# Optimization experiments

Hardware: AMD Instinct MI355X
Metric: run time of the kernel (lower is better)

## Reference

```python
import jax, jax.numpy as jnp
import numpy as np

NUM_HEADS = 12
HEAD_DIM = 64
DIM = 768
ATTN_DIM = 768
SEQ = 4096


def _rotate_half(t):
    # split last dim in halves: (x1, x2) -> (-x2, x1)
    x1, x2 = jnp.split(t, 2, axis=-1)
    return jnp.concatenate([-x2, x1], axis=-1)


def _apply_rope(t, freqs):
    # t: [B,H,L,d], freqs: [1,1,L,d]
    return t * jnp.cos(freqs) + _rotate_half(t) * jnp.sin(freqs)


def setup_inputs() -> dict:
    key = jax.random.key(0)
    ks = jax.random.split(key, 8)
    x = jax.random.normal(ks[0], (1, SEQ, DIM), dtype=jnp.float32)
    # standard rotary frequencies: theta = pos * inv_freq, concatenated twice to head_dim
    inv_freq = 1.0 / (10000.0 ** (jnp.arange(0, HEAD_DIM, 2, dtype=jnp.float32) / HEAD_DIM))
    pos = jnp.arange(SEQ, dtype=jnp.float32)
    ang = pos[:, None] * inv_freq[None, :]                      # [L, d/2]
    rope = jnp.concatenate([ang, ang], axis=-1)[None, None]     # [1,1,L,d]
    s = 0.02
    Wq = jax.random.normal(ks[1], (ATTN_DIM, DIM), dtype=jnp.float32) * s
    Wk = jax.random.normal(ks[2], (ATTN_DIM, DIM), dtype=jnp.float32) * s
    Wv = jax.random.normal(ks[3], (ATTN_DIM, DIM), dtype=jnp.float32) * s
    Wo = jax.random.normal(ks[4], (DIM, ATTN_DIM), dtype=jnp.float32) * s
    bo = jnp.zeros((DIM,), dtype=jnp.float32)
    gamma = jnp.ones((DIM,), dtype=jnp.float32)
    beta = jnp.zeros((DIM,), dtype=jnp.float32)
    return {"x": x, "Wq": Wq, "Wk": Wk, "Wv": Wv, "Wo": Wo, "bo": bo,
            "gamma": gamma, "beta": beta, "rope": rope}


def reference(x, Wq, Wk, Wv, Wo, bo, gamma, beta, rope):
    B, L, D = x.shape
    residual = x
    # pre-LayerNorm
    mu = jnp.mean(x, axis=-1, keepdims=True)
    var = jnp.mean((x - mu) ** 2, axis=-1, keepdims=True)
    xn = (x - mu) * jax.lax.rsqrt(var + 1e-5) * gamma + beta

    def heads(t):  # [B,L,attn_dim] -> [B,H,L,d]
        return t.reshape(B, L, NUM_HEADS, HEAD_DIM).transpose(0, 2, 1, 3)

    q = heads(xn @ Wq.T)
    k = heads(xn @ Wk.T)
    v = heads(xn @ Wv.T)
    q = _apply_rope(q, rope)
    k = _apply_rope(k, rope)
    v = _apply_rope(v, rope)

    scale = HEAD_DIM ** -0.5
    dots = jnp.einsum('bhid,bhjd->bhij', q, k) * scale
    # causal mask: positions j > i masked
    i = jnp.arange(L)
    mask = i[:, None] < i[None, :]  # True where future
    neg = -jnp.finfo(dots.dtype).max
    dots = jnp.where(mask[None, None], neg, dots)
    attn_map = jax.nn.softmax(dots, axis=-1)

    o = jnp.einsum('bhij,bhjd->bhid', attn_map, v)
    o = o.transpose(0, 2, 1, 3).reshape(B, L, ATTN_DIM)
    out = o @ Wo.T + bo + residual
    return out, attn_map, dots
```

## Files before the change

kernel.cpp:

```cpp
#include <hip/hip_runtime.h>
#include <hip/hip_bf16.h>
#include <cfloat>
#include <cmath>

#define SEQ 4096
#define DIM 768
#define NH 12
#define HD 64
#define NEG_MASK (-0x1.FEp+127f)

typedef __attribute__((ext_vector_type(8))) short short8_t;
typedef __attribute__((ext_vector_type(4))) float f32x4;

static __device__ __forceinline__ unsigned short f2bf(float f) {
  __hip_bfloat16 h = __float2bfloat16(f);
  unsigned short u;
  __builtin_memcpy(&u, &h, 2);
  return u;
}

static __device__ __forceinline__ void st_nt(float* p, f32x4 v) {
  __builtin_nontemporal_store(v, (f32x4*)p);
}
static __device__ __forceinline__ void st_nt1(float* p, float v) {
  __builtin_nontemporal_store(v, p);
}
static __device__ __forceinline__ f32x4 ld_lds4(const float* p) {
  return *(const f32x4*)p;
}

__global__ __launch_bounds__(256) void ln_kernel(const float* __restrict__ x,
    const float* __restrict__ gamma, const float* __restrict__ beta,
    unsigned short* __restrict__ xnb) {
  int row = blockIdx.x;
  const float* xr = x + (size_t)row * DIM;
  int t = threadIdx.x;
  float v0 = xr[t], v1 = xr[t + 256], v2 = xr[t + 512];
  float s = v0 + v1 + v2;
  float s2 = v0 * v0 + v1 * v1 + v2 * v2;
  for (int off = 32; off > 0; off >>= 1) {
    s += __shfl_down(s, off, 64);
    s2 += __shfl_down(s2, off, 64);
  }
  __shared__ float red[2][4];
  int wid = t >> 6;
  if ((t & 63) == 0) { red[0][wid] = s; red[1][wid] = s2; }
  __syncthreads();
  s = red[0][0] + red[0][1] + red[0][2] + red[0][3];
  s2 = red[1][0] + red[1][1] + red[1][2] + red[1][3];
  float mu = s * (1.0f / DIM);
  float var = s2 * (1.0f / DIM) - mu * mu;
  float rstd = rsqrtf(var + 1e-5f);
  unsigned short* xo = xnb + (size_t)row * DIM;
  xo[t]       = f2bf((v0 - mu) * rstd * gamma[t]       + beta[t]);
  xo[t + 256] = f2bf((v1 - mu) * rstd * gamma[t + 256] + beta[t + 256]);
  xo[t + 512] = f2bf((v2 - mu) * rstd * gamma[t + 512] + beta[t + 512]);
}

__global__ __launch_bounds__(256) void wcvt_kernel(const float* __restrict__ w0,
    const float* __restrict__ w1, const float* __restrict__ w2, const float* __restrict__ w3,
    unsigned short* __restrict__ o0, unsigned short* __restrict__ o1,
    unsigned short* __restrict__ o2, unsigned short* __restrict__ o3) {
  const float* src; unsigned short* dst;
  switch (blockIdx.y) {
    case 0: src = w0; dst = o0; break;
    case 1: src = w1; dst = o1; break;
    case 2: src = w2; dst = o2; break;
    default: src = w3; dst = o3; break;
  }
  size_t base = ((size_t)blockIdx.x * 256 + threadIdx.x) * 8;
  float4 a = *(const float4*)(src + base);
  float4 b = *(const float4*)(src + base + 4);
  ushort4 ua, ub;
  ua.x = f2bf(a.x); ua.y = f2bf(a.y); ua.z = f2bf(a.z); ua.w = f2bf(a.w);
  ub.x = f2bf(b.x); ub.y = f2bf(b.y); ub.z = f2bf(b.z); ub.w = f2bf(b.w);
  *(ushort4*)(dst + base) = ua;
  *(ushort4*)(dst + base + 4) = ub;
}

__global__ __launch_bounds__(256) void qkv_kernel(const unsigned short* __restrict__ xnb,
    const unsigned short* __restrict__ wqb, const unsigned short* __restrict__ wkb,
    const unsigned short* __restrict__ wvb, const float* __restrict__ ropes,
    unsigned short* __restrict__ qb, unsigned short* __restrict__ kb,
    unsigned short* __restrict__ vbT) {
  int z = blockIdx.z;
  const unsigned short* W = (z == 0) ? wqb : (z == 1) ? wkb : wvb;
  int h = blockIdx.y;
  int n0 = h * 64;
  int tid = threadIdx.x;
  int w = tid >> 6, l = tid & 63;
  int col_l = l & 15, rowg = l >> 4, kgrp = rowg * 8;
  int mbase = blockIdx.x * 64 + w * 16;

  f32x4 acc[4];
  #pragma unroll
  for (int g = 0; g < 4; g++) acc[g] = (f32x4){0.f, 0.f, 0.f, 0.f};

  for (int k0 = 0; k0 < DIM; k0 += 32) {
    short8_t a = *(const short8_t*)(xnb + (size_t)(mbase + col_l) * DIM + k0 + kgrp);
    #pragma unroll
    for (int g = 0; g < 4; g++) {
      short8_t bw = *(const short8_t*)(W + (size_t)(n0 + g * 16 + col_l) * DIM + k0 + kgrp);
      acc[g] = __builtin_amdgcn_mfma_f32_16x16x32_bf16(a, bw, acc[g], 0, 0, 0);
    }
  }

  float res[4][4];
  #pragma unroll
  for (int g = 0; g < 4; g++) {
    int d = g * 16 + col_l;
    #pragma unroll
    for (int r = 0; r < 4; r++) {
      int m = mbase + rowg * 4 + r;
      float f = ropes[(size_t)m * HD + d];
      float val = acc[g][r];
      float oth = acc[g ^ 2][r];
      float rot = (g < 2) ? -oth : oth;
      res[g][r] = val * cosf(f) + rot * sinf(f);
    }
  }

  if (z < 2) {
    unsigned short* dst = (z == 0) ? qb : kb;
    #pragma unroll
    for (int g = 0; g < 4; g++) {
      int d = g * 16 + col_l;
      #pragma unroll
      for (int r = 0; r < 4; r++)
        dst[((size_t)h * SEQ + mbase + rowg * 4 + r) * HD + d] = f2bf(res[g][r]);
    }
  } else {
    #pragma unroll
    for (int g = 0; g < 4; g++) {
      int d = g * 16 + col_l;
      ushort4 u;
      u.x = f2bf(res[g][0]); u.y = f2bf(res[g][1]);
      u.z = f2bf(res[g][2]); u.w = f2bf(res[g][3]);
      *(ushort4*)(vbT + ((size_t)h * HD + d) * SEQ + mbase + rowg * 4) = u;
    }
  }
}

__global__ __launch_bounds__(256, 4) void attn_fused(
    const unsigned short* __restrict__ qb, const unsigned short* __restrict__ kb,
    const unsigned short* __restrict__ vbT,
    float* __restrict__ dots, float* __restrict__ attnp, unsigned short* __restrict__ ob) {
  int bid = blockIdx.x;
  int g_ = (bid & 7) * 384 + (bid >> 3);
  int h = g_ >> 8;
  int band = 255 - (g_ & 255);
  int i0 = band * 16;
  int jd = i0 >> 6;
  int tid = threadIdx.x;
  int w = tid >> 6, l = tid & 63;
  int col_l = l & 15, rg = l >> 4, kgrp = rg * 8;

  const unsigned short* qh = qb + (size_t)h * SEQ * HD;
  const unsigned short* kh = kb + (size_t)h * SEQ * HD;
  const unsigned short* vh = vbT + (size_t)h * HD * SEQ;
  size_t obase = (size_t)h * SEQ * SEQ;

  __shared__ float pt[4][16][68];
  __shared__ float stats[4][16];

  const unsigned short* qrow = qh + (size_t)(i0 + col_l) * HD + kgrp;
  short8_t aq0 = *(const short8_t*)(qrow);
  short8_t aq1 = *(const short8_t*)(qrow + 32);

  float lsum[4];
  #pragma unroll
  for (int r = 0; r < 4; r++) lsum[r] = 0.f;

  for (int jt = w; jt <= jd; jt += 4) {
    int j0 = jt * 64;
    f32x4 acc[4];
    #pragma unroll
    for (int b = 0; b < 4; b++) {
      const unsigned short* kr = kh + (size_t)(j0 + b * 16 + col_l) * HD + kgrp;
      short8_t bk0 = *(const short8_t*)(kr);
      short8_t bk1 = *(const short8_t*)(kr + 32);
      f32x4 z = {0.f, 0.f, 0.f, 0.f};
      acc[b] = __builtin_amdgcn_mfma_f32_16x16x32_bf16(aq0, bk0, z, 0, 0, 0);
      acc[b] = __builtin_amdgcn_mfma_f32_16x16x32_bf16(aq1, bk1, acc[b], 0, 0, 0);
    }
    bool diag = (jt == jd);
    #pragma unroll
    for (int b = 0; b < 4; b++) {
      int j = j0 + b * 16 + col_l;
      #pragma unroll
      for (int r = 0; r < 4; r++) {
        float s = acc[b][r] * 0.125f;
        acc[b][r] = (diag && j > i0 + rg * 4 + r) ? NEG_MASK : s;
      }
    }
    #pragma unroll
    for (int r = 0; r < 4; r++) {
      lsum[r] += __expf(acc[0][r]) + __expf(acc[1][r]) +
                 __expf(acc[2][r]) + __expf(acc[3][r]);
    }
    #pragma unroll
    for (int b = 0; b < 4; b++) {
      float* dp = dots + obase + (size_t)(i0 + rg * 4) * SEQ + j0 + b * 16 + col_l;
      #pragma unroll
      for (int r = 0; r < 4; r++)
        st_nt1(dp + (size_t)r * SEQ, acc[b][r]);
    }
  }

  #pragma unroll
  for (int r = 0; r < 4; r++) {
    #pragma unroll
    for (int off = 1; off < 16; off <<= 1)
      lsum[r] += __shfl_xor(lsum[r], off, 16);
  }
  if (col_l == 0) {
    #pragma unroll
    for (int r = 0; r < 4; r++)
      stats[w][rg * 4 + r] = lsum[r];
  }
  __syncthreads();
  float rl_[4];
  #pragma unroll
  for (int r = 0; r < 4; r++) {
    int row = rg * 4 + r;
    rl_[r] = 1.0f / (stats[0][row] + stats[1][row] + stats[2][row] + stats[3][row]);
  }

  f32x4 o[4];
  #pragma unroll
  for (int dg = 0; dg < 4; dg++) o[dg] = (f32x4){0.f, 0.f, 0.f, 0.f};

  for (int jt = w; jt <= jd; jt += 4) {
    int j0 = jt * 64;
    f32x4 acc[4];
    #pragma unroll
    for (int b = 0; b < 4; b++) {
      const unsigned short* kr = kh + (size_t)(j0 + b * 16 + col_l) * HD + kgrp;
      short8_t bk0 = *(const short8_t*)(kr);
      short8_t bk1 = *(const short8_t*)(kr + 32);
      f32x4 z = {0.f, 0.f, 0.f, 0.f};
      acc[b] = __builtin_amdgcn_mfma_f32_16x16x32_bf16(aq0, bk0, z, 0, 0, 0);
      acc[b] = __builtin_amdgcn_mfma_f32_16x16x32_bf16(aq1, bk1, acc[b], 0, 0, 0);
    }
    bool diag = (jt == jd);
    #pragma unroll
    for (int b = 0; b < 4; b++) {
      int j = j0 + b * 16 + col_l;
      #pragma unroll
      for (int r = 0; r < 4; r++) {
        float s = acc[b][r] * 0.125f;
        s = (diag && j > i0 + rg * 4 + r) ? NEG_MASK : s;
        float p = __expf(s) * rl_[r];
        acc[b][r] = p;
        pt[w][rg * 4 + r][b * 16 + col_l] = p;
      }
    }
    #pragma unroll
    for (int b = 0; b < 4; b++) {
      float* ap = attnp + obase + (size_t)(i0 + rg * 4) * SEQ + j0 + b * 16 + col_l;
      #pragma unroll
      for (int r = 0; r < 4; r++)
        st_nt1(ap + (size_t)r * SEQ, acc[b][r]);
    }
    short8_t pa[2];
    #pragma unroll
    for (int ks = 0; ks < 2; ks++) {
      const float* src = &pt[w][col_l][ks * 32 + kgrp];
      f32x4 x0 = ld_lds4(src);
      f32x4 x1 = ld_lds4(src + 4);
      short8_t t;
      t[0] = (short)f2bf(x0.x); t[1] = (short)f2bf(x0.y);
      t[2] = (short)f2bf(x0.z); t[3] = (short)f2bf(x0.w);
      t[4] = (short)f2bf(x1.x); t[5] = (short)f2bf(x1.y);
      t[6] = (short)f2bf(x1.z); t[7] = (short)f2bf(x1.w);
      pa[ks] = t;
    }
    #pragma unroll
    for (int dg = 0; dg < 4; dg++) {
      const unsigned short* vr = vh + (size_t)(dg * 16 + col_l) * SEQ + j0 + kgrp;
      short8_t bv0 = *(const short8_t*)(vr);
      short8_t bv1 = *(const short8_t*)(vr + 32);
      o[dg] = __builtin_amdgcn_mfma_f32_16x16x32_bf16(pa[0], bv0, o[dg], 0, 0, 0);
      o[dg] = __builtin_amdgcn_mfma_f32_16x16x32_bf16(pa[1], bv1, o[dg], 0, 0, 0);
    }
  }

  {
    int c0 = (jd + 1) * 64;
    int nf4 = (SEQ - c0) >> 2;
    if (nf4 > 0) {
      f32x4 dm = (f32x4){NEG_MASK, NEG_MASK, NEG_MASK, NEG_MASK};
      f32x4 zz = (f32x4){0.f, 0.f, 0.f, 0.f};
      for (int r16 = 0; r16 < 16; r16++) {
        float* dr = dots  + obase + (size_t)(i0 + r16) * SEQ + c0;
        float* ar = attnp + obase + (size_t)(i0 + r16) * SEQ + c0;
        for (int c = tid; c < nf4; c += 256) {
          st_nt(dr + c * 4, dm);
          st_nt(ar + c * 4, zz);
        }
      }
    }
  }

  __syncthreads();
  #pragma unroll
  for (int dg = 0; dg < 4; dg++)
    #pragma unroll
    for (int r = 0; r < 4; r++)
      pt[w][rg * 4 + r][dg * 16 + col_l] = o[dg][r];
  __syncthreads();
  {
    int idx = tid * 4;
    int row = idx >> 6, col = idx & 63;
    f32x4 s = ld_lds4(&pt[0][row][col]);
    #pragma unroll
    for (int w2 = 1; w2 < 4; w2++) {
      f32x4 t = ld_lds4(&pt[w2][row][col]);
      s.x += t.x; s.y += t.y; s.z += t.z; s.w += t.w;
    }
    ushort4 u;
    u.x = f2bf(s.x); u.y = f2bf(s.y); u.z = f2bf(s.z); u.w = f2bf(s.w);
    *(ushort4*)(ob + (size_t)(i0 + row) * DIM + h * HD + col) = u;
  }
}

__global__ __launch_bounds__(256) void out_kernel(const unsigned short* __restrict__ ob,
    const unsigned short* __restrict__ wob, const float* __restrict__ bias,
    const float* __restrict__ resid, float* __restrict__ out) {
  int n0 = blockIdx.y * 64;
  int tid = threadIdx.x;
  int w = tid >> 6, l = tid & 63;
  int col_l = l & 15, rowg = l >> 4, kgrp = rowg * 8;
  int mbase = blockIdx.x * 64 + w * 16;

  f32x4 acc[4];
  #pragma unroll
  for (int g = 0; g < 4; g++) acc[g] = (f32x4){0.f, 0.f, 0.f, 0.f};

  for (int k0 = 0; k0 < DIM; k0 += 32) {
    short8_t a = *(const short8_t*)(ob + (size_t)(mbase + col_l) * DIM + k0 + kgrp);
    #pragma unroll
    for (int g = 0; g < 4; g++) {
      short8_t bw = *(const short8_t*)(wob + (size_t)(n0 + g * 16 + col_l) * DIM + k0 + kgrp);
      acc[g] = __builtin_amdgcn_mfma_f32_16x16x32_bf16(a, bw, acc[g], 0, 0, 0);
    }
  }
  #pragma unroll
  for (int g = 0; g < 4; g++) {
    int n = n0 + g * 16 + col_l;
    float bn = bias[n];
    #pragma unroll
    for (int r = 0; r < 4; r++) {
      int m = mbase + rowg * 4 + r;
      out[(size_t)m * DIM + n] = acc[g][r] + bn + resid[(size_t)m * DIM + n];
    }
  }
}

extern "C" void kernel_launch(void* const* d_in, const int* in_sizes, int n_in,
                              void* d_out, int out_size, void* d_ws, size_t ws_size,
                              hipStream_t stream) {
  const float* x     = (const float*)d_in[0];
  const float* Wq    = (const float*)d_in[1];
  const float* Wk    = (const float*)d_in[2];
  const float* Wv    = (const float*)d_in[3];
  const float* Wo    = (const float*)d_in[4];
  const float* bo    = (const float*)d_in[5];
  const float* gamma = (const float*)d_in[6];
  const float* beta  = (const float*)d_in[7];
  const float* rope  = (const float*)d_in[8];

  float* out  = (float*)d_out;
  float* attn = out + (size_t)SEQ * DIM;
  float* dots = attn + (size_t)NH * SEQ * SEQ;

  char* ws = (char*)d_ws;
  unsigned short* xnb = (unsigned short*)(ws);
  unsigned short* qb  = (unsigned short*)(ws + 6291456);
  unsigned short* kb  = (unsigned short*)(ws + 12582912);
  unsigned short* vbT = (unsigned short*)(ws + 18874368);
  unsigned short* ob  = (unsigned short*)(ws + 25165824);
  unsigned short* wqb = (unsigned short*)(ws + 31457280);
  unsigned short* wkb = (unsigned short*)(ws + 32636928);
  unsigned short* wvb = (unsigned short*)(ws + 33816576);
  unsigned short* wob = (unsigned short*)(ws + 34996224);

  ln_kernel<<<SEQ, 256, 0, stream>>>(x, gamma, beta, xnb);
  wcvt_kernel<<<dim3(288, 4), 256, 0, stream>>>(Wq, Wk, Wv, Wo, wqb, wkb, wvb, wob);
  qkv_kernel<<<dim3(SEQ / 64, NH, 3), 256, 0, stream>>>(xnb, wqb, wkb, wvb, rope, qb, kb, vbT);
  attn_fused<<<3072, 256, 0, stream>>>(qb, kb, vbT, dots, attn, ob);
  out_kernel<<<dim3(SEQ / 64, DIM / 64), 256, 0, stream>>>(ob, wob, bo, x, out);
}
```

Before: 585.7 us.

## Stage score tiles through LDS for vectorized stores and use 32-row bands

Before being written out, the dots and attention-probability tiles now go through LDS. Each lane reads back four consecutive columns and issues 16-byte nontemporal stores in place of scalar 4-byte stores. The attention kernel also grows to 512 threads handling 32-row bands, with two groups of four waves that share K/V tile loads across the band. This targets write-coalescing cost on the huge attention-map outputs, at the price of extra LDS traffic, a larger shared array and fewer, bigger blocks.

```diff
diff --git a/kernel.cpp b/kernel.cpp
--- a/kernel.cpp
+++ b/kernel.cpp
@@ -21,9 +21,6 @@
 
 static __device__ __forceinline__ void st_nt(float* p, f32x4 v) {
   __builtin_nontemporal_store(v, (f32x4*)p);
-}
-static __device__ __forceinline__ void st_nt1(float* p, float v) {
-  __builtin_nontemporal_store(v, p);
 }
 static __device__ __forceinline__ f32x4 ld_lds4(const float* p) {
   return *(const f32x4*)p;
@@ -141,29 +138,32 @@
   }
 }
 
-__global__ __launch_bounds__(256, 4) void attn_fused(
+__global__ __launch_bounds__(512, 4) void attn_fused(
     const unsigned short* __restrict__ qb, const unsigned short* __restrict__ kb,
     const unsigned short* __restrict__ vbT,
     float* __restrict__ dots, float* __restrict__ attnp, unsigned short* __restrict__ ob) {
   int bid = blockIdx.x;
-  int g_ = (bid & 7) * 384 + (bid >> 3);
-  int h = g_ >> 8;
-  int band = 255 - (g_ & 255);
-  int i0 = band * 16;
+  int g_ = (bid & 7) * 192 + (bid >> 3);
+  int h = g_ / 128;
+  int band = 127 - (g_ & 127);
+  int i0 = band * 32;
   int jd = i0 >> 6;
   int tid = threadIdx.x;
   int w = tid >> 6, l = tid & 63;
+  int g = w >> 2, s = w & 3;
   int col_l = l & 15, rg = l >> 4, kgrp = rg * 8;
+  int c4 = col_l * 4;
+  int r0 = i0 + g * 16;
 
   const unsigned short* qh = qb + (size_t)h * SEQ * HD;
   const unsigned short* kh = kb + (size_t)h * SEQ * HD;
   const unsigned short* vh = vbT + (size_t)h * HD * SEQ;
   size_t obase = (size_t)h * SEQ * SEQ;
 
-  __shared__ float pt[4][16][68];
-  __shared__ float stats[4][16];
-
-  const unsigned short* qrow = qh + (size_t)(i0 + col_l) * HD + kgrp;
+  __shared__ float pt[8][16][68];
+  __shared__ float stats[8][16];
+
+  const unsigned short* qrow = qh + (size_t)(r0 + col_l) * HD + kgrp;
   short8_t aq0 = *(const short8_t*)(qrow);
   short8_t aq1 = *(const short8_t*)(qrow + 32);
 
@@ -171,7 +171,7 @@
   #pragma unroll
   for (int r = 0; r < 4; r++) lsum[r] = 0.f;
 
-  for (int jt = w; jt <= jd; jt += 4) {
+  for (int jt = s; jt <= jd; jt += 4) {
     int j0 = jt * 64;
     f32x4 acc[4];
     #pragma unroll
@@ -189,8 +189,8 @@
       int j = j0 + b * 16 + col_l;
       #pragma unroll
       for (int r = 0; r < 4; r++) {
-        float s = acc[b][r] * 0.125f;
-        acc[b][r] = (diag && j > i0 + rg * 4 + r) ? NEG_MASK : s;
+        float sv = acc[b][r] * 0.125f;
+        acc[b][r] = (diag && j > r0 + rg * 4 + r) ? NEG_MASK : sv;
       }
     }
     #pragma unroll
@@ -199,11 +199,14 @@
                  __expf(acc[2][r]) + __expf(acc[3][r]);
     }
     #pragma unroll
-    for (int b = 0; b < 4; b++) {
-      float* dp = dots + obase + (size_t)(i0 + rg * 4) * SEQ + j0 + b * 16 + col_l;
+    for (int b = 0; b < 4; b++)
       #pragma unroll
       for (int r = 0; r < 4; r++)
-        st_nt1(dp + (size_t)r * SEQ, acc[b][r]);
+        pt[w][rg * 4 + r][b * 16 + col_l] = acc[b][r];
+    #pragma unroll
+    for (int e = 0; e < 4; e++) {
+      f32x4 v = ld_lds4(&pt[w][e * 4 + rg][c4]);
+      st_nt(dots + obase + (size_t)(r0 + e * 4 + rg) * SEQ + j0 + c4, v);
     }
   }
 
@@ -223,14 +226,15 @@
   #pragma unroll
   for (int r = 0; r < 4; r++) {
     int row = rg * 4 + r;
-    rl_[r] = 1.0f / (stats[0][row] + stats[1][row] + stats[2][row] + stats[3][row]);
+    rl_[r] = 1.0f / (stats[g * 4 + 0][row] + stats[g * 4 + 1][row] +
+                     stats[g * 4 + 2][row] + stats[g * 4 + 3][row]);
   }
 
   f32x4 o[4];
   #pragma unroll
   for (int dg = 0; dg < 4; dg++) o[dg] = (f32x4){0.f, 0.f, 0.f, 0.f};
 
-  for (int jt = w; jt <= jd; jt += 4) {
+  for (int jt = s; jt <= jd; jt += 4) {
     int j0 = jt * 64;
     f32x4 acc[4];
     #pragma unroll
@@ -248,19 +252,16 @@
       int j = j0 + b * 16 + col_l;
       #pragma unroll
       for (int r = 0; r < 4; r++) {
-        float s = acc[b][r] * 0.125f;
-        s = (diag && j > i0 + rg * 4 + r) ? NEG_MASK : s;
-        float p = __expf(s) * rl_[r];
-        acc[b][r] = p;
+        float sv = acc[b][r] * 0.125f;
+        sv = (diag && j > r0 + rg * 4 + r) ? NEG_MASK : sv;
+        float p = __expf(sv) * rl_[r];
         pt[w][rg * 4 + r][b * 16 + col_l] = p;
       }
     }
     #pragma unroll
-    for (int b = 0; b < 4; b++) {
-      float* ap = attnp + obase + (size_t)(i0 + rg * 4) * SEQ + j0 + b * 16 + col_l;
-      #pragma unroll
-      for (int r = 0; r < 4; r++)
-        st_nt1(ap + (size_t)r * SEQ, acc[b][r]);
+    for (int e = 0; e < 4; e++) {
+      f32x4 v = ld_lds4(&pt[w][e * 4 + rg][c4]);
+      st_nt(attnp + obase + (size_t)(r0 + e * 4 + rg) * SEQ + j0 + c4, v);
     }
     short8_t pa[2];
     #pragma unroll
@@ -291,10 +292,10 @@
     if (nf4 > 0) {
       f32x4 dm = (f32x4){NEG_MASK, NEG_MASK, NEG_MASK, NEG_MASK};
       f32x4 zz = (f32x4){0.f, 0.f, 0.f, 0.f};
-      for (int r16 = 0; r16 < 16; r16++) {
-        float* dr = dots  + obase + (size_t)(i0 + r16) * SEQ + c0;
-        float* ar = attnp + obase + (size_t)(i0 + r16) * SEQ + c0;
-        for (int c = tid; c < nf4; c += 256) {
+      for (int r32 = 0; r32 < 32; r32++) {
+        float* dr = dots  + obase + (size_t)(i0 + r32) * SEQ + c0;
+        float* ar = attnp + obase + (size_t)(i0 + r32) * SEQ + c0;
+        for (int c = tid; c < nf4; c += 512) {
           st_nt(dr + c * 4, dm);
           st_nt(ar + c * 4, zz);
         }
@@ -311,16 +312,17 @@
   __syncthreads();
   {
     int idx = tid * 4;
-    int row = idx >> 6, col = idx & 63;
-    f32x4 s = ld_lds4(&pt[0][row][col]);
-    #pragma unroll
-    for (int w2 = 1; w2 < 4; w2++) {
-      f32x4 t = ld_lds4(&pt[w2][row][col]);
-      s.x += t.x; s.y += t.y; s.z += t.z; s.w += t.w;
+    int g2 = idx >> 10, rem = idx & 1023;
+    int row = rem >> 6, col = rem & 63;
+    f32x4 sv = ld_lds4(&pt[g2 * 4][row][col]);
+    #pragma unroll
+    for (int s2 = 1; s2 < 4; s2++) {
+      f32x4 t = ld_lds4(&pt[g2 * 4 + s2][row][col]);
+      sv.x += t.x; sv.y += t.y; sv.z += t.z; sv.w += t.w;
     }
     ushort4 u;
-    u.x = f2bf(s.x); u.y = f2bf(s.y); u.z = f2bf(s.z); u.w = f2bf(s.w);
-    *(ushort4*)(ob + (size_t)(i0 + row) * DIM + h * HD + col) = u;
+    u.x = f2bf(sv.x); u.y = f2bf(sv.y); u.z = f2bf(sv.z); u.w = f2bf(sv.w);
+    *(ushort4*)(ob + (size_t)(i0 + g2 * 16 + row) * DIM + h * HD + col) = u;
   }
 }
 
@@ -388,6 +390,6 @@
   ln_kernel<<<SEQ, 256, 0, stream>>>(x, gamma, beta, xnb);
   wcvt_kernel<<<dim3(288, 4), 256, 0, stream>>>(Wq, Wk, Wv, Wo, wqb, wkb, wvb, wob);
   qkv_kernel<<<dim3(SEQ / 64, NH, 3), 256, 0, stream>>>(xnb, wqb, wkb, wvb, rope, qb, kb, vbT);
-  attn_fused<<<3072, 256, 0, stream>>>(qb, kb, vbT, dots, attn, ob);
+  attn_fused<<<1536, 512, 0, stream>>>(qb, kb, vbT, dots, attn, ob);
   out_kernel<<<dim3(SEQ / 64, DIM / 64), 256, 0, stream>>>(ob, wob, bo, x, out);
 }
```

After: 573.9 us. 2.0% less time.
